# Performance work log

Hardware: AMD Instinct MI355X
Metric: run time of the kernel (lower is better)

## Reference

```python
import jax, jax.numpy as jnp
import numpy as np

B, T, D = 2, 2048, 2048
H, G, HD = 16, 4, 128
SCALE = 0.08838834764831845  # 1/sqrt(head_dim)
THETA = 10000.0
EPS = 1e-10


def _rope(x):
    # x: [B, T, h, HD]; faithful to source: cos/sin built from cat([freqs, freqs])
    hd = x.shape[-1]
    pos = jnp.arange(x.shape[1], dtype=x.dtype)
    inv_freq = 1.0 / (THETA ** (jnp.arange(0, hd, 2, dtype=x.dtype) / hd))
    freqs = pos[:, None] * inv_freq[None, :]            # [T, hd/2]
    emb = jnp.concatenate([freqs, freqs], axis=-1)      # [T, hd]
    cos = jnp.cos(emb)[None, :, None, :]
    sin = jnp.sin(emb)[None, :, None, :]
    x_even, x_odd = x[..., ::2], x[..., 1::2]
    rotated = jnp.stack((-x_odd, x_even), axis=-1).reshape(x.shape)
    return x * cos + rotated * sin


def _qk_norm(x):
    # F.normalize(p=2): x / clamp_min(||x||, eps)
    n = jnp.sqrt(jnp.sum(x * x, axis=-1, keepdims=True))
    return x / jnp.maximum(n, EPS)


def setup_inputs() -> dict:
    key = jax.random.key(0)
    k1, k2, k3 = jax.random.split(key, 3)
    x = jax.random.normal(k1, (B, T, D), dtype=jnp.float32)
    w_qkv = jax.random.normal(k2, (H * HD + 2 * G * HD, D), dtype=jnp.float32) * 0.02
    w_o = jax.random.normal(k3, (D, D), dtype=jnp.float32) * 0.02
    padding_mask = jnp.ones((B, T), dtype=bool)
    return {"x": x, "w_qkv": w_qkv, "w_o": w_o, "padding_mask": padding_mask,
            "use_qk_norm": 1, "use_mqa": 0}


def reference(x, w_qkv, w_o, padding_mask, use_qk_norm, use_mqa):
    qkv = jnp.einsum('btd,ed->bte', x, w_qkv)           # fused QKV projection
    q = qkv[..., :H * HD].reshape(B, T, H, HD)
    k = qkv[..., H * HD:H * HD + G * HD].reshape(B, T, G, HD)
    v = qkv[..., H * HD + G * HD:].reshape(B, T, G, HD)
    if use_qk_norm:
        q = _qk_norm(q)
        k = _qk_norm(k)
    q = _rope(q)
    k = _rope(k)
    if not use_mqa:
        rep = H // G
        k = jnp.repeat(k, rep, axis=2)                  # [B, T, H, HD]
        v = jnp.repeat(v, rep, axis=2)
    # attention: scores [B, H, Tq, Tk]
    scores = jnp.einsum('bqhd,bkhd->bhqk', q, k) * SCALE
    # faithful mask expansion: padding_mask[:, None, :, None] -> [B,1,Tq,Tk]
    mask = padding_mask[:, None, :, None]
    scores = jnp.where(mask, scores, jnp.finfo(scores.dtype).min)
    attn = jax.nn.softmax(scores, axis=-1)
    out = jnp.einsum('bhqk,bkhd->bqhd', attn, v).reshape(B, T, D)
    return jnp.einsum('btd,od->bto', out, w_o)
```

## Files before the change

kernel.cpp:

```cpp
#include <hip/hip_runtime.h>
#include <hip/hip_bf16.h>
#include <math.h>

#define B_SZ 2
#define T_SEQ 2048
#define D_MODEL 2048
#define NH 16
#define NG 4
#define HD 128
#define E_QKV 3072
#define SCALE_F 0.08838834764831845f

typedef __attribute__((ext_vector_type(8))) short short8;
typedef __attribute__((ext_vector_type(8))) _Float16 half8;
typedef __attribute__((ext_vector_type(4))) float f32x4;
typedef __attribute__((ext_vector_type(16))) float f32x16;
typedef __attribute__((ext_vector_type(4))) uint uint4v;

__device__ inline ushort f2bf(float f) {
    union { float f; uint u; } v; v.f = f;
    uint r = (v.u + 0x7FFFu + ((v.u >> 16) & 1u)) >> 16;
    return (ushort)r;
}
__device__ inline ushort f2h(float f) {
    union { _Float16 h; ushort u; } v;
    v.h = (_Float16)f;
    return v.u;
}

__device__ inline void glds16(const void* g, void* l) {
    __builtin_amdgcn_global_load_lds(
        (const __attribute__((address_space(1))) unsigned int*)g,
        (__attribute__((address_space(3))) unsigned int*)l,
        16, 0, 0);
}

__device__ inline uint cvtpk(float a, float b) {
    uint r;
    asm("v_cvt_pk_bf16_f32 %0, %1, %2" : "=v"(r) : "v"(a), "v"(b));
    return r;
}
__device__ inline void pl32swap(uint& a, uint& b) {
    asm("v_permlane32_swap_b32 %0, %1" : "+v"(a), "+v"(b));
}

__global__ __launch_bounds__(256) void prepass(const float* __restrict__ x,
                                               const float* __restrict__ wq,
                                               const float* __restrict__ wo,
                                               ushort* __restrict__ x16,
                                               ushort* __restrict__ wq16,
                                               ushort* __restrict__ wo16,
                                               float2* __restrict__ Rt,
                                               int n4x, int n4q, int n4o) {
    int i = blockIdx.x * 256 + threadIdx.x;
    const int ncvt = n4x + n4q + n4o;
    if (i < ncvt) {
        const float* src;
        ushort* dst;
        if (i < n4x)            { src = x;  dst = x16; }
        else if (i < n4x + n4q) { src = wq; dst = wq16; i -= n4x; }
        else                    { src = wo; dst = wo16; i -= n4x + n4q; }
        float4 v = ((const float4*)src)[i];
        uint2 ho;
        ho.x = (uint)f2h(v.x) | ((uint)f2h(v.y) << 16);
        ho.y = (uint)f2h(v.z) | ((uint)f2h(v.w) << 16);
        ((uint2*)dst)[i] = ho;
        return;
    }
    int r = i - ncvt;
    if (r >= T_SEQ * 64) return;
    int t = r >> 6, j = r & 63;
    float inv_freq = exp2f(-0.2076205059304595f * (float)j);
    float sn, cs;
    sincosf((float)t * inv_freq, &sn, &cs);
    Rt[r] = make_float2(cs, sn);
}

template <bool QKV>
__global__ __launch_bounds__(256, 3)
void gemm_f16(const ushort* __restrict__ A,
              const ushort* __restrict__ B,
              float* __restrict__ C,
              ushort* __restrict__ Qb,
              ushort* __restrict__ Kb,
              ushort* __restrict__ Vt,
              const float2* __restrict__ Rt,
              int M, int N, int K) {
    __shared__ __attribute__((aligned(16))) ushort smem[16384];
    ushort* sA = smem;
    ushort* sB = smem + 8192;

    const int tid  = threadIdx.x;
    const int wave = tid >> 6;
    const int lane = tid & 63;
    const int c    = lane & 15;
    const int quad = lane >> 4;
    const int wr   = wave >> 1;
    const int wc   = wave & 1;
    const size_t m0 = (size_t)blockIdx.y * 128;
    const size_t n0 = (size_t)blockIdx.x * 128;

    const int srow = lane >> 3;
    const int sg   = ((lane & 7) ^ (srow & 7)) * 8;
    const ushort* gsrc;
    ushort* sdst;
    if (wave < 2) {
        gsrc = A + (m0 + wave * 64 + srow) * (size_t)K + sg;
        sdst = sA + wave * 4096;
    } else {
        gsrc = B + (n0 + (wave - 2) * 64 + srow) * (size_t)K + sg;
        sdst = sB + (wave - 2) * 4096;
    }

    f32x4 acc[4][4];
#pragma unroll
    for (int i = 0; i < 4; ++i)
#pragma unroll
        for (int j = 0; j < 4; ++j) acc[i][j] = (f32x4){0.f, 0.f, 0.f, 0.f};

    const int cg = c & 7;

    for (int k0 = 0; k0 < K; k0 += 64) {
        if (k0) __syncthreads();
#pragma unroll
        for (int i = 0; i < 8; ++i)
            glds16(gsrc + (size_t)(i * 8) * K + k0, sdst + i * 512);
        __syncthreads();

#pragma unroll
        for (int ks = 0; ks < 2; ++ks) {
            const int ga = ((ks * 4 + quad) ^ cg) * 8;
            half8 fa[4];
#pragma unroll
            for (int mi = 0; mi < 4; ++mi)
                fa[mi] = *(const half8*)&sA[(wr * 64 + mi * 16 + c) * 64 + ga];
#pragma unroll
            for (int ni = 0; ni < 4; ++ni) {
                half8 fb = *(const half8*)&sB[(wc * 64 + ni * 16 + c) * 64 + ga];
#pragma unroll
                for (int mi = 0; mi < 4; ++mi)
                    acc[mi][ni] = __builtin_amdgcn_mfma_f32_16x16x32_f16(fa[mi], fb, acc[mi][ni], 0, 0, 0);
            }
        }
    }

    if constexpr (!QKV) {
#pragma unroll
        for (int mi = 0; mi < 4; ++mi)
#pragma unroll
            for (int ni = 0; ni < 4; ++ni)
#pragma unroll
                for (int r = 0; r < 4; ++r)
                    C[(m0 + wr * 64 + mi * 16 + quad * 4 + r) * N + n0 + wc * 64 + ni * 16 + c] =
                        acc[mi][ni][r];
        return;
    } else {
        const int hq = blockIdx.x;
        const int gmBase = (int)m0 + wr * 64;
        __syncthreads();

        if (hq < NH + NG) {
            float ps[4][4];
#pragma unroll
            for (int mi = 0; mi < 4; ++mi)
#pragma unroll
                for (int r = 0; r < 4; ++r) {
                    float s = 0.f;
#pragma unroll
                    for (int ni = 0; ni < 4; ++ni) {
                        float v = acc[mi][ni][r];
                        s += v * v;
                    }
#pragma unroll
                    for (int o = 1; o < 16; o <<= 1) s += __shfl_xor(s, o);
                    ps[mi][r] = s;
                }
            float* red = (float*)smem;
            if (c == 0) {
#pragma unroll
                for (int mi = 0; mi < 4; ++mi)
#pragma unroll
                    for (int r = 0; r < 4; ++r)
                        red[wave * 64 + mi * 16 + quad * 4 + r] = ps[mi][r];
            }
            __syncthreads();

            const int hb = (hq < NH) ? hq : hq - NH;

#pragma unroll
            for (int mi = 0; mi < 4; ++mi)
#pragma unroll
                for (int r = 0; r < 4; ++r) {
                    const int rid = mi * 16 + quad * 4 + r;
                    float s2 = red[wave * 64 + rid] + red[(wave ^ 1) * 64 + rid];
                    float inv = 1.f / fmaxf(sqrtf(s2), 1e-10f);
                    const int gm = gmBase + rid;
                    const int b = gm >> 11, t = gm & (T_SEQ - 1);
                    const float2* rt = Rt + (size_t)t * 64;
#pragma unroll
                    for (int ni = 0; ni < 4; ++ni) {
                        float nx = acc[mi][ni][r] * inv;
                        float2 cs2 = rt[ni * 16 + c];
                        float nb = __shfl_xor(nx, 1);
                        float rot = (c & 1) ? nb : -nb;
                        float val = nx * cs2.x + rot * cs2.y;
                        const int d = wc * 64 + ni * 16 + c;
                        if (hq < NH)
                            Qb[(((size_t)b * NH + hb) * T_SEQ + t) * HD + d] = f2bf(val * SCALE_F);
                        else
                            Kb[(((size_t)b * NG + hb) * T_SEQ + t) * HD + d] = f2bf(val);
                    }
                }
        } else {
            const int g  = hq - (NH + NG);
            const int b  = (int)(m0 >> 11);
            const int t0 = (int)(m0 & (T_SEQ - 1));
            const int bg = b * NG + g;
            const int dd = wave * 32 + (lane >> 1);
            const int th = lane & 1;
#pragma unroll
            for (int pass = 0; pass < 2; ++pass) {
                if (wr == pass) {
#pragma unroll
                    for (int mi = 0; mi < 4; ++mi)
#pragma unroll
                        for (int ni = 0; ni < 4; ++ni) {
                            uint2 w;
                            w.x = cvtpk(acc[mi][ni][0], acc[mi][ni][1]);
                            w.y = cvtpk(acc[mi][ni][2], acc[mi][ni][3]);
                            const int d  = wc * 64 + ni * 16 + c;
                            const int tl = mi * 16 + quad * 4;
                            *(uint2*)&smem[d * 72 + tl] = w;
                        }
                }
                __syncthreads();
                size_t vb = ((size_t)bg * HD + dd) * T_SEQ + t0 + pass * 64 + th * 32;
#pragma unroll
                for (int k = 0; k < 4; ++k) {
                    short8 v = *(const short8*)&smem[dd * 72 + th * 32 + k * 8];
                    *(short8*)&Vt[vb + k * 8] = v;
                }
                __syncthreads();
            }
        }
    }
}

__global__ __launch_bounds__(256, 2) void attn_mfma5(const ushort* __restrict__ Qb,
                                                     const ushort* __restrict__ Kb,
                                                     const ushort* __restrict__ Vt,
                                                     ushort* __restrict__ AOh) {
    __shared__ __attribute__((aligned(16))) ushort Ks[2][64 * 128];
    __shared__ __attribute__((aligned(16))) ushort Vts[2][128 * 64 + 128];

    const int qt   = blockIdx.x;
    const int h    = blockIdx.y;
    const int b    = blockIdx.z;
    const int g    = h >> 2;
    const int tid  = threadIdx.x;
    const int wave = tid >> 6;
    const int lane = tid & 63;
    const int l31  = lane & 31;
    const int hi   = lane >> 5;
    const int wq   = wave * 32;

    const ushort* Qg = Qb + (((size_t)b * NH + h) * T_SEQ + qt * 128) * HD;
    const ushort* Kg = Kb + ((size_t)b * NG + g) * T_SEQ * HD;
    const ushort* Vg = Vt + ((size_t)b * NG + g) * (size_t)HD * T_SEQ;

    int goK[8];
#pragma unroll
    for (int s = 0; s < 8; ++s) goK[s] = ((2 * s + hi) ^ (l31 & 15)) * 8;
    int vbase[4];
#pragma unroll
    for (int db = 0; db < 4; ++db)
        vbase[db] = (db * 32 + l31) * 64 + (db * 4 + (l31 >> 3)) * 8;
    int goV[4];
#pragma unroll
    for (int s4 = 0; s4 < 4; ++s4) goV[s4] = ((2 * s4 + hi) ^ (l31 & 7)) * 8;

    auto stage = [&](int buf, int kt) {
#pragma unroll
        for (int i = 0; i < 4; ++i) {
            int row = wave * 16 + i * 4 + (lane >> 4);
            glds16(Kg + (size_t)(kt + row) * HD + (((lane & 15) ^ (row & 15)) * 8),
                   &Ks[buf][(wave * 16 + i * 4) * 128]);
        }
#pragma unroll
        for (int i = 0; i < 4; ++i) {
            int row = wave * 32 + i * 8 + (lane >> 3);
            int iss = wave * 4 + i;
            glds16(Vg + (size_t)row * T_SEQ + kt + (((lane & 7) ^ (row & 7)) * 8),
                   &Vts[buf][(size_t)iss * 520]);
        }
    };

    stage(0, 0);

    short8 qf[8];
#pragma unroll
    for (int s = 0; s < 8; ++s)
        qf[s] = *(const short8*)&Qg[(size_t)(wq + l31) * HD + s * 16 + hi * 8];

    f32x16 O[4];
#pragma unroll
    for (int i = 0; i < 4; ++i)
#pragma unroll
        for (int r = 0; r < 16; ++r) O[i][r] = 0.f;
    float lp = 0.f;

    __syncthreads();

    for (int t = 0; t < T_SEQ / 64; ++t) {
        const int cur = t & 1;
        if (t + 1 < T_SEQ / 64) stage(cur ^ 1, (t + 1) * 64);

        const ushort* KsC = Ks[cur];
        const ushort* VtC = Vts[cur];

        f32x16 S0, S1;
#pragma unroll
        for (int r = 0; r < 16; ++r) { S0[r] = 0.f; S1[r] = 0.f; }

        __builtin_amdgcn_s_setprio(1);

#pragma unroll
        for (int s = 0; s < 8; ++s) {
            short8 kf0 = *(const short8*)&KsC[l31 * 128 + goK[s]];
            S0 = __builtin_amdgcn_mfma_f32_32x32x16_bf16(kf0, qf[s], S0, 0, 0, 0);
        }

        float p0[16];
#pragma unroll
        for (int s = 0; s < 8; ++s) {
            short8 kf1 = *(const short8*)&KsC[(32 + l31) * 128 + goK[s]];
            S1 = __builtin_amdgcn_mfma_f32_32x32x16_bf16(kf1, qf[s], S1, 0, 0, 0);
            p0[2 * s]     = __expf(S0[2 * s]);     lp += p0[2 * s];
            p0[2 * s + 1] = __expf(S0[2 * s + 1]); lp += p0[2 * s + 1];
        }
        short8 pa[4];
        {
            uint c0 = cvtpk(p0[0], p0[1]),   c1 = cvtpk(p0[2], p0[3]);
            uint c2 = cvtpk(p0[4], p0[5]),   c3 = cvtpk(p0[6], p0[7]);
            uint c4 = cvtpk(p0[8], p0[9]),   c5 = cvtpk(p0[10], p0[11]);
            uint c6 = cvtpk(p0[12], p0[13]), c7 = cvtpk(p0[14], p0[15]);
            pl32swap(c0, c2); pl32swap(c1, c3);
            pl32swap(c4, c6); pl32swap(c5, c7);
            union { uint4v u; short8 s8; } ua, ub;
            ua.u = (uint4v){c0, c1, c2, c3};
            ub.u = (uint4v){c4, c5, c6, c7};
            pa[0] = ua.s8; pa[1] = ub.s8;
        }

        float p1[16];
#pragma unroll
        for (int j = 0; j < 8; ++j) {
            const int s4 = j >> 2;
            const int db = j & 3;
            short8 vf = *(const short8*)&VtC[vbase[db] + goV[s4]];
            O[db] = __builtin_amdgcn_mfma_f32_32x32x16_bf16(pa[s4], vf, O[db], 0, 0, 0);
            p1[2 * j]     = __expf(S1[2 * j]);     lp += p1[2 * j];
            p1[2 * j + 1] = __expf(S1[2 * j + 1]); lp += p1[2 * j + 1];
        }
        {
            uint c0 = cvtpk(p1[0], p1[1]),   c1 = cvtpk(p1[2], p1[3]);
            uint c2 = cvtpk(p1[4], p1[5]),   c3 = cvtpk(p1[6], p1[7]);
            uint c4 = cvtpk(p1[8], p1[9]),   c5 = cvtpk(p1[10], p1[11]);
            uint c6 = cvtpk(p1[12], p1[13]), c7 = cvtpk(p1[14], p1[15]);
            pl32swap(c0, c2); pl32swap(c1, c3);
            pl32swap(c4, c6); pl32swap(c5, c7);
            union { uint4v u; short8 s8; } ua, ub;
            ua.u = (uint4v){c0, c1, c2, c3};
            ub.u = (uint4v){c4, c5, c6, c7};
            pa[2] = ua.s8; pa[3] = ub.s8;
        }

#pragma unroll
        for (int j = 0; j < 8; ++j) {
            const int s4 = 2 + (j >> 2);
            const int db = j & 3;
            short8 vf = *(const short8*)&VtC[vbase[db] + goV[s4]];
            O[db] = __builtin_amdgcn_mfma_f32_32x32x16_bf16(pa[s4], vf, O[db], 0, 0, 0);
        }
        __builtin_amdgcn_s_setprio(0);

        __syncthreads();
    }

    lp += __shfl_xor(lp, 32);
    float inv = 1.f / lp;
#pragma unroll
    for (int r = 0; r < 16; ++r) {
        int qp = (r & 3) + 8 * (r >> 2) + 4 * hi;
        float iv = __shfl(inv, qp);
        size_t idx = ((size_t)b * T_SEQ + qt * 128 + wq + qp) * D_MODEL + h * HD + l31;
#pragma unroll
        for (int db = 0; db < 4; ++db)
            AOh[idx + db * 32] = f2h(O[db][r] * iv);
    }
}

extern "C" void kernel_launch(void* const* d_in, const int* in_sizes, int n_in,
                              void* d_out, int out_size, void* d_ws, size_t ws_size,
                              hipStream_t stream) {
    const float* x      = (const float*)d_in[0];
    const float* w_qkv  = (const float*)d_in[1];
    const float* w_o    = (const float*)d_in[2];

    float* out = (float*)d_out;

    const int M = B_SZ * T_SEQ;
    const size_t nX  = (size_t)M * D_MODEL;
    const size_t nWq = (size_t)E_QKV * D_MODEL;
    const size_t nWo = (size_t)D_MODEL * D_MODEL;

    ushort* x16  = (ushort*)d_ws;
    ushort* aoh  = x16 + nX;
    ushort* wq16 = aoh + nX;
    ushort* wo16 = wq16 + nWq;
    ushort* Qb   = wo16 + nWo;
    ushort* Kb   = Qb + (size_t)B_SZ * NH * T_SEQ * HD;
    ushort* Vt   = Kb + (size_t)B_SZ * NG * T_SEQ * HD;
    float2* Rt   = (float2*)(Vt + (size_t)B_SZ * NG * (size_t)HD * T_SEQ);

    {
        int n4x = (int)(nX / 4), n4q = (int)(nWq / 4), n4o = (int)(nWo / 4);
        int ntot = n4x + n4q + n4o + T_SEQ * 64;
        prepass<<<(ntot + 255) / 256, 256, 0, stream>>>(x, w_qkv, w_o,
                                                        x16, wq16, wo16, Rt,
                                                        n4x, n4q, n4o);
    }

    {
        dim3 grid(E_QKV / 128, M / 128);
        gemm_f16<true><<<grid, 256, 0, stream>>>(x16, wq16,
                                                 nullptr, Qb, Kb, Vt, Rt,
                                                 M, E_QKV, D_MODEL);
    }
    {
        dim3 grid(T_SEQ / 128, NH, B_SZ);
        attn_mfma5<<<grid, 256, 0, stream>>>(Qb, Kb, Vt, aoh);
    }
    {
        dim3 grid(D_MODEL / 128, M / 128);
        gemm_f16<false><<<grid, 256, 0, stream>>>(aoh, wo16,
                                                  out, nullptr, nullptr, nullptr, nullptr,
                                                  M, D_MODEL, D_MODEL);
    }
}
```

Baseline: 192.7 us.

## Software-pipeline attention loop: overlap PV of previous tile with QK of current

Restructures the attention main loop into a prologue, a steady-state loop and an epilogue. The P·V MFMAs for tile t-1 are interleaved with the Q·K MFMAs and the exp of tile t. V fragments are preloaded into registers (16 short8) before the barrier. The aim is to hide the serial dependency between exp/softmax and the PV matmul and keep the matrix units busy. In exchange it raises register pressure with vreg plus the carried pa, which under launch_bounds(256,2) could cause spills.

```diff
diff --git a/kernel.cpp b/kernel.cpp
--- a/kernel.cpp
+++ b/kernel.cpp
@@ -246,7 +246,7 @@
     }
 }
 
-__global__ __launch_bounds__(256, 2) void attn_mfma5(const ushort* __restrict__ Qb,
+__global__ __launch_bounds__(256, 2) void attn_mfma6(const ushort* __restrict__ Qb,
                                                      const ushort* __restrict__ Kb,
                                                      const ushort* __restrict__ Vt,
                                                      ushort* __restrict__ AOh) {
@@ -309,36 +309,29 @@
         for (int r = 0; r < 16; ++r) O[i][r] = 0.f;
     float lp = 0.f;
 
+    short8 pa[4];
+    short8 vreg[16];
+
     __syncthreads();
 
-    for (int t = 0; t < T_SEQ / 64; ++t) {
-        const int cur = t & 1;
-        if (t + 1 < T_SEQ / 64) stage(cur ^ 1, (t + 1) * 64);
-
-        const ushort* KsC = Ks[cur];
-        const ushort* VtC = Vts[cur];
-
+    {
+        stage(1, 64);
+        const ushort* KsC = Ks[0];
         f32x16 S0, S1;
 #pragma unroll
         for (int r = 0; r < 16; ++r) { S0[r] = 0.f; S1[r] = 0.f; }
-
         __builtin_amdgcn_s_setprio(1);
-
 #pragma unroll
         for (int s = 0; s < 8; ++s) {
             short8 kf0 = *(const short8*)&KsC[l31 * 128 + goK[s]];
+            short8 kf1 = *(const short8*)&KsC[(32 + l31) * 128 + goK[s]];
             S0 = __builtin_amdgcn_mfma_f32_32x32x16_bf16(kf0, qf[s], S0, 0, 0, 0);
-        }
-
+            S1 = __builtin_amdgcn_mfma_f32_32x32x16_bf16(kf1, qf[s], S1, 0, 0, 0);
+        }
+        __builtin_amdgcn_s_setprio(0);
         float p0[16];
 #pragma unroll
-        for (int s = 0; s < 8; ++s) {
-            short8 kf1 = *(const short8*)&KsC[(32 + l31) * 128 + goK[s]];
-            S1 = __builtin_amdgcn_mfma_f32_32x32x16_bf16(kf1, qf[s], S1, 0, 0, 0);
-            p0[2 * s]     = __expf(S0[2 * s]);     lp += p0[2 * s];
-            p0[2 * s + 1] = __expf(S0[2 * s + 1]); lp += p0[2 * s + 1];
-        }
-        short8 pa[4];
+        for (int r = 0; r < 16; ++r) { p0[r] = __expf(S0[r]); lp += p0[r]; }
         {
             uint c0 = cvtpk(p0[0], p0[1]),   c1 = cvtpk(p0[2], p0[3]);
             uint c2 = cvtpk(p0[4], p0[5]),   c3 = cvtpk(p0[6], p0[7]);
@@ -351,17 +344,9 @@
             ub.u = (uint4v){c4, c5, c6, c7};
             pa[0] = ua.s8; pa[1] = ub.s8;
         }
-
         float p1[16];
 #pragma unroll
-        for (int j = 0; j < 8; ++j) {
-            const int s4 = j >> 2;
-            const int db = j & 3;
-            short8 vf = *(const short8*)&VtC[vbase[db] + goV[s4]];
-            O[db] = __builtin_amdgcn_mfma_f32_32x32x16_bf16(pa[s4], vf, O[db], 0, 0, 0);
-            p1[2 * j]     = __expf(S1[2 * j]);     lp += p1[2 * j];
-            p1[2 * j + 1] = __expf(S1[2 * j + 1]); lp += p1[2 * j + 1];
-        }
+        for (int r = 0; r < 16; ++r) { p1[r] = __expf(S1[r]); lp += p1[r]; }
         {
             uint c0 = cvtpk(p1[0], p1[1]),   c1 = cvtpk(p1[2], p1[3]);
             uint c2 = cvtpk(p1[4], p1[5]),   c3 = cvtpk(p1[6], p1[7]);
@@ -374,18 +359,88 @@
             ub.u = (uint4v){c4, c5, c6, c7};
             pa[2] = ua.s8; pa[3] = ub.s8;
         }
-
+        const ushort* VtC = Vts[0];
+#pragma unroll
+        for (int s4 = 0; s4 < 4; ++s4)
+#pragma unroll
+            for (int db = 0; db < 4; ++db)
+                vreg[s4 * 4 + db] = *(const short8*)&VtC[vbase[db] + goV[s4]];
+        __syncthreads();
+    }
+
+    for (int t = 1; t < T_SEQ / 64; ++t) {
+        const int cur = t & 1;
+        if (t + 1 < T_SEQ / 64) stage(cur ^ 1, (t + 1) * 64);
+
+        const ushort* KsC = Ks[cur];
+
+        f32x16 S0, S1;
+#pragma unroll
+        for (int r = 0; r < 16; ++r) { S0[r] = 0.f; S1[r] = 0.f; }
+
+        __builtin_amdgcn_s_setprio(1);
+#pragma unroll
+        for (int s = 0; s < 8; ++s) {
+            short8 kf0 = *(const short8*)&KsC[l31 * 128 + goK[s]];
+            S0 = __builtin_amdgcn_mfma_f32_32x32x16_bf16(kf0, qf[s], S0, 0, 0, 0);
+            short8 kf1 = *(const short8*)&KsC[(32 + l31) * 128 + goK[s]];
+            S1 = __builtin_amdgcn_mfma_f32_32x32x16_bf16(kf1, qf[s], S1, 0, 0, 0);
+            O[s & 3] = __builtin_amdgcn_mfma_f32_32x32x16_bf16(pa[s >> 2], vreg[(s >> 2) * 4 + (s & 3)], O[s & 3], 0, 0, 0);
+        }
+        float p0[16];
 #pragma unroll
         for (int j = 0; j < 8; ++j) {
-            const int s4 = 2 + (j >> 2);
-            const int db = j & 3;
-            short8 vf = *(const short8*)&VtC[vbase[db] + goV[s4]];
-            O[db] = __builtin_amdgcn_mfma_f32_32x32x16_bf16(pa[s4], vf, O[db], 0, 0, 0);
+            O[j & 3] = __builtin_amdgcn_mfma_f32_32x32x16_bf16(pa[2 + (j >> 2)], vreg[(2 + (j >> 2)) * 4 + (j & 3)], O[j & 3], 0, 0, 0);
+            p0[2 * j]     = __expf(S0[2 * j]);     lp += p0[2 * j];
+            p0[2 * j + 1] = __expf(S0[2 * j + 1]); lp += p0[2 * j + 1];
         }
         __builtin_amdgcn_s_setprio(0);
 
+        {
+            uint c0 = cvtpk(p0[0], p0[1]),   c1 = cvtpk(p0[2], p0[3]);
+            uint c2 = cvtpk(p0[4], p0[5]),   c3 = cvtpk(p0[6], p0[7]);
+            uint c4 = cvtpk(p0[8], p0[9]),   c5 = cvtpk(p0[10], p0[11]);
+            uint c6 = cvtpk(p0[12], p0[13]), c7 = cvtpk(p0[14], p0[15]);
+            pl32swap(c0, c2); pl32swap(c1, c3);
+            pl32swap(c4, c6); pl32swap(c5, c7);
+            union { uint4v u; short8 s8; } ua, ub;
+            ua.u = (uint4v){c0, c1, c2, c3};
+            ub.u = (uint4v){c4, c5, c6, c7};
+            pa[0] = ua.s8; pa[1] = ub.s8;
+        }
+        float p1[16];
+#pragma unroll
+        for (int r = 0; r < 16; ++r) { p1[r] = __expf(S1[r]); lp += p1[r]; }
+        {
+            uint c0 = cvtpk(p1[0], p1[1]),   c1 = cvtpk(p1[2], p1[3]);
+            uint c2 = cvtpk(p1[4], p1[5]),   c3 = cvtpk(p1[6], p1[7]);
+            uint c4 = cvtpk(p1[8], p1[9]),   c5 = cvtpk(p1[10], p1[11]);
+            uint c6 = cvtpk(p1[12], p1[13]), c7 = cvtpk(p1[14], p1[15]);
+            pl32swap(c0, c2); pl32swap(c1, c3);
+            pl32swap(c4, c6); pl32swap(c5, c7);
+            union { uint4v u; short8 s8; } ua, ub;
+            ua.u = (uint4v){c0, c1, c2, c3};
+            ub.u = (uint4v){c4, c5, c6, c7};
+            pa[2] = ua.s8; pa[3] = ub.s8;
+        }
+
+        const ushort* VtC = Vts[cur];
+#pragma unroll
+        for (int s4 = 0; s4 < 4; ++s4)
+#pragma unroll
+            for (int db = 0; db < 4; ++db)
+                vreg[s4 * 4 + db] = *(const short8*)&VtC[vbase[db] + goV[s4]];
+
         __syncthreads();
     }
+
+    __builtin_amdgcn_s_setprio(1);
+#pragma unroll
+    for (int s4 = 0; s4 < 4; ++s4)
+#pragma unroll
+        for (int db = 0; db < 4; ++db)
+            O[db] = __builtin_amdgcn_mfma_f32_32x32x16_bf16(pa[s4], vreg[s4 * 4 + db], O[db], 0, 0, 0);
+    __builtin_amdgcn_s_setprio(0);
 
     lp += __shfl_xor(lp, 32);
     float inv = 1.f / lp;
@@ -439,7 +494,7 @@
     }
     {
         dim3 grid(T_SEQ / 128, NH, B_SZ);
-        attn_mfma5<<<grid, 256, 0, stream>>>(Qb, Kb, Vt, aoh);
+        attn_mfma6<<<grid, 256, 0, stream>>>(Qb, Kb, Vt, aoh);
     }
     {
         dim3 grid(D_MODEL / 128, M / 128);
```

Result: no change. 194.3 us (+0.8%).
